# Kernel tuning notes

Measured on AMD Instinct MI355X. Metric: run time of the kernel, lower is better.

Reference implementation:

```python
import jax, jax.numpy as jnp
import numpy as np

N, D = 4096, 32


def setup_inputs() -> dict:
    key = jax.random.key(0)
    k1, _ = jax.random.split(key)
    particles = jax.random.normal(k1, (N, D), dtype=jnp.float32)
    length_scale = jnp.ones((1,), dtype=jnp.float32)
    return {"particles": particles, "length_scale": length_scale}


def reference(particles, length_scale):
    # SVGDModel.calculate_gradient with an RBF kernel and standard-Gaussian density.
    num_particles = particles.shape[0]
    ls2 = length_scale[0] ** 2

    # pairwise differences: diff[i, j] = x_i - x_j  -> [N, N, D]
    diff = particles[:, None, :] - particles[None, :, :]
    sq_dists = jnp.sum(diff * diff, axis=-1)               # [N, N]

    # gram_matrix = k(x_i, x_j) = exp(-||x_i - x_j||^2 / (2 l^2))
    gram_matrix = jnp.exp(-sq_dists / (2.0 * ls2))          # [N, N]

    # density.score for standard Gaussian: grad log p(x) = -x
    score_matrix = -particles                               # [N, D]

    # kernel_gradient[i, j] = grad_{x_i} k(x_i, x_j) = -(x_i - x_j)/l^2 * k
    kernel_gradient = -(diff / ls2) * gram_matrix[..., None]  # [N, N, D]

    kernel_score_term = jnp.einsum('ij,jk->ik', gram_matrix, score_matrix)  # [N, D]
    kernel_gradient_term = jnp.sum(kernel_gradient, axis=0)                 # [N, D]

    phi = (kernel_score_term + kernel_gradient_term) / num_particles
    return phi
```

## Files before the change

kernel.cpp:

```cpp
#include <hip/hip_runtime.h>

#define NPART 4096
#define DIM 32
#define LOG2E 1.44269504088896340736f
#define SHSTR 36

typedef _Float16 f16x8 __attribute__((ext_vector_type(8)));
typedef _Float16 f16x4 __attribute__((ext_vector_type(4)));
typedef float f32x4 __attribute__((ext_vector_type(4)));

__global__ __launch_bounds__(256, 4) void svgd_onepass_kernel(
    const float* __restrict__ X, const float* __restrict__ ls,
    float* __restrict__ out) {
  __shared__ __align__(16) unsigned char smem[28672];
  _Float16* sHi = (_Float16*)smem;
  _Float16* sLo = (_Float16*)(smem + 9216);
  _Float16* sXT = (_Float16*)(smem + 18432);
  float* sM2 = (float*)(smem + 27136);
  float* sS = (float*)(smem + 28160);
  float* sT = (float*)smem;

  const int tid = threadIdx.x;
  const int lane = tid & 63;
  const int g = lane >> 4;
  const int li = lane & 15;
  const int wave = tid >> 6;
  const int i0 = blockIdx.x * 32;
  const int jb0 = blockIdx.y * 512;

  const float lsv = ls[0];
  const float inv = 1.f / (lsv * lsv);
  const float si2 = LOG2E * inv;
  const float hm = 0.5f * si2;

  const float4* X4 = (const float4*)X;

  f16x8 bh0, bl0, bh1, bl1;
  float mi0, mi1;
  {
    const int r0 = i0 + li, r1 = i0 + 16 + li;
    float4 a0 = X4[(size_t)r0 * 8 + g], b0 = X4[(size_t)r0 * 8 + 4 + g];
    float4 a1 = X4[(size_t)r1 * 8 + g], b1 = X4[(size_t)r1 * 8 + 4 + g];
    float t0[8] = {a0.x, a0.y, a0.z, a0.w, b0.x, b0.y, b0.z, b0.w};
    float t1[8] = {a1.x, a1.y, a1.z, a1.w, b1.x, b1.y, b1.z, b1.w};
    float n0 = 0.f, n1 = 0.f;
#pragma unroll
    for (int e = 0; e < 8; ++e) {
      n0 = fmaf(t0[e], t0[e], n0);
      n1 = fmaf(t1[e], t1[e], n1);
      _Float16 h0 = (_Float16)t0[e];
      _Float16 h1 = (_Float16)t1[e];
      bh0[e] = h0; bl0[e] = (_Float16)(t0[e] - (float)h0);
      bh1[e] = h1; bl1[e] = (_Float16)(t1[e] - (float)h1);
    }
    n0 += __shfl_xor(n0, 16, 64);
    n0 += __shfl_xor(n0, 32, 64);
    n1 += __shfl_xor(n1, 16, 64);
    n1 += __shfl_xor(n1, 32, 64);
    mi0 = n0 * hm;
    mi1 = n1 * hm;
  }

  f32x4 c2a0 = {0.f, 0.f, 0.f, 0.f}, c2b0 = {0.f, 0.f, 0.f, 0.f};
  f32x4 c2a1 = {0.f, 0.f, 0.f, 0.f}, c2b1 = {0.f, 0.f, 0.f, 0.f};
  float Sp0 = 0.f, Sp1 = 0.f;

#pragma unroll
  for (int s = 0; s < 4; ++s) {
    __syncthreads();
    {
      const int r = tid >> 1, sub = tid & 1;
      const int row = jb0 + s * 128 + r;
      const float4* src = X4 + (size_t)row * 8 + sub * 4;
      float4 va = src[0], vb = src[1], vc = src[2], vd = src[3];
      float tv[16] = {va.x, va.y, va.z, va.w, vb.x, vb.y, vb.z, vb.w,
                      vc.x, vc.y, vc.z, vc.w, vd.x, vd.y, vd.z, vd.w};
      _Float16 h[16], l[16];
      float nrm = 0.f;
#pragma unroll
      for (int e = 0; e < 16; ++e) {
        nrm = fmaf(tv[e], tv[e], nrm);
        _Float16 hh = (_Float16)tv[e];
        h[e] = hh;
        l[e] = (_Float16)(tv[e] - (float)hh);
      }
      sM2[sub * 128 + r] = nrm * hm;
#pragma unroll
      for (int gq = 0; gq < 4; ++gq) {
        f16x4 ph, pl;
#pragma unroll
        for (int e = 0; e < 4; ++e) { ph[e] = h[4 * gq + e]; pl[e] = l[4 * gq + e]; }
        *(f16x4*)(sHi + r * SHSTR + gq * 8 + sub * 4) = ph;
        *(f16x4*)(sLo + r * SHSTR + gq * 8 + sub * 4) = pl;
      }
#pragma unroll
      for (int e = 0; e < 16; ++e) sXT[(16 * sub + e) * 136 + r] = h[e];
    }
    __syncthreads();

#pragma unroll
    for (int it = 0; it < 2; ++it) {
      const int jloc = wave * 32 + it * 16;
      const _Float16* hb = sHi + (jloc + li) * SHSTR + g * 8;
      const _Float16* lb = sLo + (jloc + li) * SHSTR + g * 8;
      f16x4 AhL = *(const f16x4*)(hb);
      f16x4 AhH = *(const f16x4*)(hb + 4);
      f16x4 AlL = *(const f16x4*)(lb);
      f16x4 AlH = *(const f16x4*)(lb + 4);
      f16x8 Ah = __builtin_shufflevector(AhL, AhH, 0, 1, 2, 3, 4, 5, 6, 7);
      f16x8 Al = __builtin_shufflevector(AlL, AlH, 0, 1, 2, 3, 4, 5, 6, 7);
      f16x4 Ba = *(const f16x4*)(sXT + li * 136 + jloc + 4 * g);
      f16x4 Bb = *(const f16x4*)(sXT + (16 + li) * 136 + jloc + 4 * g);
      f32x4 Mja = *(const f32x4*)(sM2 + jloc + 4 * g);
      f32x4 Mjb = *(const f32x4*)(sM2 + 128 + jloc + 4 * g);

      f32x4 c10 = {0.f, 0.f, 0.f, 0.f}, c11 = {0.f, 0.f, 0.f, 0.f};
      c10 = __builtin_amdgcn_mfma_f32_16x16x32_f16(Ah, bh0, c10, 0, 0, 0);
      c11 = __builtin_amdgcn_mfma_f32_16x16x32_f16(Ah, bh1, c11, 0, 0, 0);
      c10 = __builtin_amdgcn_mfma_f32_16x16x32_f16(Al, bh0, c10, 0, 0, 0);
      c11 = __builtin_amdgcn_mfma_f32_16x16x32_f16(Al, bh1, c11, 0, 0, 0);
      c10 = __builtin_amdgcn_mfma_f32_16x16x32_f16(Ah, bl0, c10, 0, 0, 0);
      c11 = __builtin_amdgcn_mfma_f32_16x16x32_f16(Ah, bl1, c11, 0, 0, 0);
      f16x4 a20, a21;
#pragma unroll
      for (int r = 0; r < 4; ++r) {
        const float mj = Mja[r] + Mjb[r];
        float k0 = exp2f(fmaf(c10[r], si2, -(mi0 + mj)));
        float k1 = exp2f(fmaf(c11[r], si2, -(mi1 + mj)));
        Sp0 += k0;
        Sp1 += k1;
        a20[r] = (_Float16)k0;
        a21[r] = (_Float16)k1;
      }
      c2a0 = __builtin_amdgcn_mfma_f32_16x16x16f16(a20, Ba, c2a0, 0, 0, 0);
      c2b0 = __builtin_amdgcn_mfma_f32_16x16x16f16(a20, Bb, c2b0, 0, 0, 0);
      c2a1 = __builtin_amdgcn_mfma_f32_16x16x16f16(a21, Ba, c2a1, 0, 0, 0);
      c2b1 = __builtin_amdgcn_mfma_f32_16x16x16f16(a21, Bb, c2b1, 0, 0, 0);
    }
  }

  __syncthreads();

#pragma unroll
  for (int r = 0; r < 4; ++r) {
    sT[(wave * 32 + 4 * g + r) * 32 + li] = c2a0[r];
    sT[(wave * 32 + 4 * g + r) * 32 + 16 + li] = c2b0[r];
    sT[(wave * 32 + 16 + 4 * g + r) * 32 + li] = c2a1[r];
    sT[(wave * 32 + 16 + 4 * g + r) * 32 + 16 + li] = c2b1[r];
  }
  {
    float s0 = Sp0, s1 = Sp1;
    s0 += __shfl_xor(s0, 16, 64);
    s0 += __shfl_xor(s0, 32, 64);
    s1 += __shfl_xor(s1, 16, 64);
    s1 += __shfl_xor(s1, 32, 64);
    if (g == 0) {
      sS[wave * 32 + li] = s0;
      sS[wave * 32 + 16 + li] = s1;
    }
  }
  __syncthreads();

  const float c1f = inv * (1.f / NPART);
  const float c2f = (1.f + inv) * (1.f / NPART);
#pragma unroll
  for (int q = 0; q < 4; ++q) {
    const int v = q * 256 + tid;
    const int row = v >> 5, d = v & 31;
    const float T = sT[(0 * 32 + row) * 32 + d] + sT[(1 * 32 + row) * 32 + d] +
                    sT[(2 * 32 + row) * 32 + d] + sT[(3 * 32 + row) * 32 + d];
    const float S = sS[0 * 32 + row] + sS[1 * 32 + row] + sS[2 * 32 + row] +
                    sS[3 * 32 + row];
    const size_t idx = (size_t)(i0 + row) * DIM + d;
    unsafeAtomicAdd(&out[idx], c1f * S * X[idx] - c2f * T);
  }
}

#define TJ 64
__global__ __launch_bounds__(256) void svgd_direct_kernel(const float* __restrict__ X,
                                                          const float* __restrict__ ls,
                                                          float* __restrict__ out) {
  __shared__ float4 sX[TJ * 8];
  const int tid = threadIdx.x;
  const int row = blockIdx.x * 256 + tid;
  const float lsv = ls[0];
  const float ls2 = lsv * lsv;
  const float inv2 = 0.5f / ls2;
  float4 xi[8];
  const float4* xr = reinterpret_cast<const float4*>(X + (size_t)row * DIM);
#pragma unroll
  for (int q = 0; q < 8; ++q) xi[q] = xr[q];
  float4 acc[8];
#pragma unroll
  for (int q = 0; q < 8; ++q) acc[q] = make_float4(0.f, 0.f, 0.f, 0.f);
  float S = 0.f;
  for (int jb = 0; jb < NPART; jb += TJ) {
    __syncthreads();
    const float4* src = reinterpret_cast<const float4*>(X + (size_t)jb * DIM);
    for (int t = tid; t < TJ * 8; t += 256) sX[t] = src[t];
    __syncthreads();
    for (int t = 0; t < TJ; ++t) {
      const float4* xj = &sX[t * 8];
      float4 v[8];
      float d0 = 0.f, d1 = 0.f, d2 = 0.f, d3 = 0.f;
#pragma unroll
      for (int q = 0; q < 8; ++q) {
        v[q] = xj[q];
        float ax = xi[q].x - v[q].x; d0 = fmaf(ax, ax, d0);
        float ay = xi[q].y - v[q].y; d1 = fmaf(ay, ay, d1);
        float az = xi[q].z - v[q].z; d2 = fmaf(az, az, d2);
        float aw = xi[q].w - v[q].w; d3 = fmaf(aw, aw, d3);
      }
      float k = __expf(-((d0 + d1) + (d2 + d3)) * inv2);
      S += k;
#pragma unroll
      for (int q = 0; q < 8; ++q) {
        acc[q].x = fmaf(k, v[q].x, acc[q].x);
        acc[q].y = fmaf(k, v[q].y, acc[q].y);
        acc[q].z = fmaf(k, v[q].z, acc[q].z);
        acc[q].w = fmaf(k, v[q].w, acc[q].w);
      }
    }
  }
  const float inv = 1.f / ls2;
  const float c1 = inv * S;
  const float c2 = 1.f + inv;
  float4* o = reinterpret_cast<float4*>(out + (size_t)row * DIM);
#pragma unroll
  for (int q = 0; q < 8; ++q) {
    float4 r;
    r.x = (c1 * xi[q].x - c2 * acc[q].x) * (1.f / NPART);
    r.y = (c1 * xi[q].y - c2 * acc[q].y) * (1.f / NPART);
    r.z = (c1 * xi[q].z - c2 * acc[q].z) * (1.f / NPART);
    r.w = (c1 * xi[q].w - c2 * acc[q].w) * (1.f / NPART);
    o[q] = r;
  }
}

extern "C" void kernel_launch(void* const* d_in, const int* in_sizes, int n_in,
                              void* d_out, int out_size, void* d_ws, size_t ws_size,
                              hipStream_t stream) {
  const float* X = (const float*)d_in[0];
  const float* ls = (const float*)d_in[1];
  float* out = (float*)d_out;
  (void)d_ws;
  (void)ws_size;

  hipError_t e =
      hipMemsetAsync(d_out, 0, (size_t)out_size * sizeof(float), stream);
  if (e == hipSuccess) {
    dim3 grid(NPART / 32, 8);
    svgd_onepass_kernel<<<grid, 256, 0, stream>>>(X, ls, out);
    return;
  }
  svgd_direct_kernel<<<NPART / 256, 256, 0, stream>>>(X, ls, out);
}
```

Before: 25.93 us.

## Halve j-tile staging size to shrink LDS and simplify per-row norm computation

Stages 64 rows per step instead of 128 and loops 8 times instead of 4, cutting shared memory from 28 KB to about 17 KB so more blocks can be resident per CU. Each row is loaded by 4 threads with two float4 loads, and the squared norm is reduced with shuffles into a single sM2 entry. This removes the two-partial norm sum. The stage loop is no longer unrolled and adds twice as many barriers, which may offset the occupancy gain.

```diff
diff --git a/kernel.cpp b/kernel.cpp
--- a/kernel.cpp
+++ b/kernel.cpp
@@ -12,13 +12,13 @@
 __global__ __launch_bounds__(256, 4) void svgd_onepass_kernel(
     const float* __restrict__ X, const float* __restrict__ ls,
     float* __restrict__ out) {
-  __shared__ __align__(16) unsigned char smem[28672];
+  __shared__ __align__(16) unsigned char smem[16896];
   _Float16* sHi = (_Float16*)smem;
-  _Float16* sLo = (_Float16*)(smem + 9216);
-  _Float16* sXT = (_Float16*)(smem + 18432);
-  float* sM2 = (float*)(smem + 27136);
-  float* sS = (float*)(smem + 28160);
+  _Float16* sLo = (_Float16*)(smem + 4608);
+  _Float16* sXT = (_Float16*)(smem + 9216);
+  float* sM2 = (float*)(smem + 13824);
   float* sT = (float*)smem;
+  float* sS = (float*)(smem + 16384);
 
   const int tid = threadIdx.x;
   const int lane = tid & 63;
@@ -65,42 +65,44 @@
   f32x4 c2a1 = {0.f, 0.f, 0.f, 0.f}, c2b1 = {0.f, 0.f, 0.f, 0.f};
   float Sp0 = 0.f, Sp1 = 0.f;
 
-#pragma unroll
-  for (int s = 0; s < 4; ++s) {
+  for (int s = 0; s < 8; ++s) {
     __syncthreads();
     {
-      const int r = tid >> 1, sub = tid & 1;
-      const int row = jb0 + s * 128 + r;
-      const float4* src = X4 + (size_t)row * 8 + sub * 4;
-      float4 va = src[0], vb = src[1], vc = src[2], vd = src[3];
-      float tv[16] = {va.x, va.y, va.z, va.w, vb.x, vb.y, vb.z, vb.w,
-                      vc.x, vc.y, vc.z, vc.w, vd.x, vd.y, vd.z, vd.w};
-      _Float16 h[16], l[16];
+      const int r = tid >> 2, ss = tid & 3;
+      const int row = jb0 + s * 64 + r;
+      float4 a = X4[(size_t)row * 8 + ss];
+      float4 b = X4[(size_t)row * 8 + 4 + ss];
+      float tv[8] = {a.x, a.y, a.z, a.w, b.x, b.y, b.z, b.w};
+      _Float16 h[8];
+      f16x4 pl0, pl1;
       float nrm = 0.f;
 #pragma unroll
-      for (int e = 0; e < 16; ++e) {
+      for (int e = 0; e < 8; ++e) {
         nrm = fmaf(tv[e], tv[e], nrm);
         _Float16 hh = (_Float16)tv[e];
         h[e] = hh;
-        l[e] = (_Float16)(tv[e] - (float)hh);
-      }
-      sM2[sub * 128 + r] = nrm * hm;
-#pragma unroll
-      for (int gq = 0; gq < 4; ++gq) {
-        f16x4 ph, pl;
-#pragma unroll
-        for (int e = 0; e < 4; ++e) { ph[e] = h[4 * gq + e]; pl[e] = l[4 * gq + e]; }
-        *(f16x4*)(sHi + r * SHSTR + gq * 8 + sub * 4) = ph;
-        *(f16x4*)(sLo + r * SHSTR + gq * 8 + sub * 4) = pl;
-      }
-#pragma unroll
-      for (int e = 0; e < 16; ++e) sXT[(16 * sub + e) * 136 + r] = h[e];
-    }
-    __syncthreads();
-
-#pragma unroll
-    for (int it = 0; it < 2; ++it) {
-      const int jloc = wave * 32 + it * 16;
+        _Float16 ll = (_Float16)(tv[e] - (float)hh);
+        if (e < 4) pl0[e] = ll; else pl1[e - 4] = ll;
+      }
+      f16x4 ph0 = {h[0], h[1], h[2], h[3]};
+      f16x4 ph1 = {h[4], h[5], h[6], h[7]};
+      *(f16x4*)(sHi + r * SHSTR + ss * 8) = ph0;
+      *(f16x4*)(sHi + r * SHSTR + ss * 8 + 4) = ph1;
+      *(f16x4*)(sLo + r * SHSTR + ss * 8) = pl0;
+      *(f16x4*)(sLo + r * SHSTR + ss * 8 + 4) = pl1;
+#pragma unroll
+      for (int e = 0; e < 8; ++e) {
+        const int d = (e < 4) ? (4 * ss + e) : (16 + 4 * ss + (e - 4));
+        sXT[d * 72 + r] = h[e];
+      }
+      nrm += __shfl_xor(nrm, 1, 64);
+      nrm += __shfl_xor(nrm, 2, 64);
+      if (ss == 0) sM2[r] = nrm * hm;
+    }
+    __syncthreads();
+
+    {
+      const int jloc = wave * 16;
       const _Float16* hb = sHi + (jloc + li) * SHSTR + g * 8;
       const _Float16* lb = sLo + (jloc + li) * SHSTR + g * 8;
       f16x4 AhL = *(const f16x4*)(hb);
@@ -109,10 +111,9 @@
       f16x4 AlH = *(const f16x4*)(lb + 4);
       f16x8 Ah = __builtin_shufflevector(AhL, AhH, 0, 1, 2, 3, 4, 5, 6, 7);
       f16x8 Al = __builtin_shufflevector(AlL, AlH, 0, 1, 2, 3, 4, 5, 6, 7);
-      f16x4 Ba = *(const f16x4*)(sXT + li * 136 + jloc + 4 * g);
-      f16x4 Bb = *(const f16x4*)(sXT + (16 + li) * 136 + jloc + 4 * g);
-      f32x4 Mja = *(const f32x4*)(sM2 + jloc + 4 * g);
-      f32x4 Mjb = *(const f32x4*)(sM2 + 128 + jloc + 4 * g);
+      f16x4 Ba = *(const f16x4*)(sXT + li * 72 + jloc + 4 * g);
+      f16x4 Bb = *(const f16x4*)(sXT + (16 + li) * 72 + jloc + 4 * g);
+      f32x4 Mj = *(const f32x4*)(sM2 + jloc + 4 * g);
 
       f32x4 c10 = {0.f, 0.f, 0.f, 0.f}, c11 = {0.f, 0.f, 0.f, 0.f};
       c10 = __builtin_amdgcn_mfma_f32_16x16x32_f16(Ah, bh0, c10, 0, 0, 0);
@@ -124,9 +125,8 @@
       f16x4 a20, a21;
 #pragma unroll
       for (int r = 0; r < 4; ++r) {
-        const float mj = Mja[r] + Mjb[r];
-        float k0 = exp2f(fmaf(c10[r], si2, -(mi0 + mj)));
-        float k1 = exp2f(fmaf(c11[r], si2, -(mi1 + mj)));
+        float k0 = exp2f(fmaf(c10[r], si2, -(mi0 + Mj[r])));
+        float k1 = exp2f(fmaf(c11[r], si2, -(mi1 + Mj[r])));
         Sp0 += k0;
         Sp1 += k1;
         a20[r] = (_Float16)k0;
```

Measured after the change: 25.65 us, median of 2. Within noise of the previous version (-1.1%).
